# Performance work log

Hardware: AMD Instinct MI355X
Metric: run time of the kernel (lower is better)

Reference implementation:

```python
import jax, jax.numpy as jnp
import numpy as np

N = 50000
E = 800000
IN_C = 128
HID = 16
HEADS = 8
OUT_C = 64
NEG_SLOPE = 0.2


def setup_inputs() -> dict:
    key = jax.random.key(0)
    ks = jax.random.split(key, 12)
    x = jax.random.normal(ks[0], (N, IN_C), dtype=jnp.float32)
    edge_index = jax.random.randint(ks[1], (2, E), 0, N, dtype=jnp.int32)
    s = 0.1
    W1 = jax.random.normal(ks[2], (IN_C, HEADS * HID), dtype=jnp.float32) * s
    a1_src = jax.random.normal(ks[3], (HEADS, HID), dtype=jnp.float32) * s
    a1_dst = jax.random.normal(ks[4], (HEADS, HID), dtype=jnp.float32) * s
    b1 = jnp.zeros((HEADS * HID,), dtype=jnp.float32)
    W2 = jax.random.normal(ks[5], (HEADS * HID, OUT_C), dtype=jnp.float32) * s
    a2_src = jax.random.normal(ks[6], (1, OUT_C), dtype=jnp.float32) * s
    a2_dst = jax.random.normal(ks[7], (1, OUT_C), dtype=jnp.float32) * s
    b2 = jnp.zeros((OUT_C,), dtype=jnp.float32)
    return {"x": x, "edge_index": edge_index, "W1": W1, "a1_src": a1_src,
            "a1_dst": a1_dst, "b1": b1, "W2": W2, "a2_src": a2_src,
            "a2_dst": a2_dst, "b2": b2}


def gat_conv(x, src, dst, W, a_src, a_dst, b, heads, ch):
    # linear projection -> [N, H, C]
    h = (x @ W).reshape(N, heads, ch)
    # per-node attention logits [N, H]
    al_s = jnp.einsum('nhc,hc->nh', h, a_src)
    al_d = jnp.einsum('nhc,hc->nh', h, a_dst)
    # per-edge logits [E, H]
    e = jax.nn.leaky_relu(al_s[src] + al_d[dst], NEG_SLOPE)
    # segment softmax over incoming edges of each dst node
    emax = jax.ops.segment_max(e, dst, num_segments=N)
    ee = jnp.exp(e - emax[dst])
    denom = jax.ops.segment_sum(ee, dst, num_segments=N)
    alpha = ee / (denom[dst] + 1e-16)
    # weighted scatter-aggregate of source messages
    msg = h[src] * alpha[:, :, None]  # [E, H, C]
    out = jax.ops.segment_sum(msg, dst, num_segments=N)
    return out.reshape(N, heads * ch) + b


def reference(x, edge_index, W1, a1_src, a1_dst, b1, W2, a2_src, a2_dst, b2):
    # add self loops (PyG GATConv default add_self_loops=True)
    loops = jnp.arange(N, dtype=edge_index.dtype)
    src = jnp.concatenate([edge_index[0], loops])
    dst = jnp.concatenate([edge_index[1], loops])
    h = gat_conv(x, src, dst, W1, a1_src, a1_dst, b1, HEADS, HID)
    h = jax.nn.relu(h)
    # dropout p=0.6 is identity in eval mode
    out = gat_conv(h, src, dst, W2, a2_src, a2_dst, b2, 1, OUT_C)
    return out
```

## Files before the change

kernel.cpp:

```cpp
#include <hip/hip_runtime.h>
#include <hip/hip_fp16.h>
#include <math.h>

#define N_NODES 50000
#define E_EDGES 800000
#define IN_C    128
#define HID     16
#define HEADS   8
#define OUT_C   64
#define NEG_SLOPE 0.2f
#define ELLW    64

template <int OUTC, int HEADS_T>
__global__ __launch_bounds__(256) void fused_gemm_fill(
    const float* __restrict__ X, const float* __restrict__ W, __half* __restrict__ H,
    const float* __restrict__ a_src, const float* __restrict__ a_dst,
    float* __restrict__ als, float* __restrict__ ald, int nrows,
    const int* __restrict__ src, const int* __restrict__ dst,
    int* __restrict__ cursor, int* __restrict__ ell) {
    constexpr int CPG = OUTC / 4;
    constexpr int RT = (256 / CPG) * 4;
    constexpr int GROUP = (OUTC / HEADS_T) / 4;
    __shared__ __half wsh[IN_C * OUTC];
    __shared__ float xs[RT * 132];
    const int bid = blockIdx.x;

    if (bid & 1) {
        const int tid = (bid >> 1) * 256 + threadIdx.x;
        if (tid < E_EDGES / 4) {
            const int4 s4 = ((const int4*)src)[tid];
            const int4 d4 = ((const int4*)dst)[tid];
            const int p0 = atomicAdd(&cursor[d4.x], 1);
            const int p1 = atomicAdd(&cursor[d4.y], 1);
            const int p2 = atomicAdd(&cursor[d4.z], 1);
            const int p3 = atomicAdd(&cursor[d4.w], 1);
            ell[(size_t)d4.x * ELLW + p0] = s4.x;
            ell[(size_t)d4.y * ELLW + p1] = s4.y;
            ell[(size_t)d4.z * ELLW + p2] = s4.z;
            ell[(size_t)d4.w * ELLW + p3] = s4.w;
        }
        return;
    }

    const int t = threadIdx.x;
    for (int f = t * 4; f < IN_C * OUTC; f += 1024) {
        const float4 w4 = *(const float4*)&W[f];
        *(__half2*)&wsh[f]     = __float22half2_rn(make_float2(w4.x, w4.y));
        *(__half2*)&wsh[f + 2] = __float22half2_rn(make_float2(w4.z, w4.w));
    }
    const int row0 = (bid >> 1) * 64;
    const int cp = t % CPG;
    const int r0 = (t / CPG) * 4;
    float asr[4], adr[4];
#pragma unroll
    for (int j = 0; j < 4; ++j) {
        asr[j] = a_src[cp * 4 + j];
        adr[j] = a_dst[cp * 4 + j];
    }
    for (int rb = 0; rb < 64; rb += RT) {
        __syncthreads();
        for (int f = t * 4; f < RT * IN_C; f += 1024) {
            const int r = f >> 7, k = f & 127;
            int rl = row0 + rb + r;
            if (rl >= nrows) rl = nrows - 1;
            *(float4*)&xs[r * 132 + k] = *(const float4*)&X[(size_t)rl * IN_C + k];
        }
        __syncthreads();
        float acc[4][4] = {};
#pragma unroll 8
        for (int k = 0; k < IN_C; ++k) {
            const float2 wlo = __half22float2(*(const __half2*)&wsh[k * OUTC + cp * 4]);
            const float2 whi = __half22float2(*(const __half2*)&wsh[k * OUTC + cp * 4 + 2]);
#pragma unroll
            for (int i = 0; i < 4; ++i) {
                const float xi = xs[(r0 + i) * 132 + k];
                acc[i][0] += xi * wlo.x;
                acc[i][1] += xi * wlo.y;
                acc[i][2] += xi * whi.x;
                acc[i][3] += xi * whi.y;
            }
        }
#pragma unroll
        for (int i = 0; i < 4; ++i) {
            const int r = row0 + rb + r0 + i;
            float ps = acc[i][0] * asr[0] + acc[i][1] * asr[1] +
                       acc[i][2] * asr[2] + acc[i][3] * asr[3];
            float pd = acc[i][0] * adr[0] + acc[i][1] * adr[1] +
                       acc[i][2] * adr[2] + acc[i][3] * adr[3];
#pragma unroll
            for (int off = 1; off < GROUP; off <<= 1) {
                ps += __shfl_xor(ps, off);
                pd += __shfl_xor(pd, off);
            }
            if (r < nrows) {
                __half* hp = H + (size_t)r * OUTC + cp * 4;
                *(__half2*)(hp)     = __float22half2_rn(make_float2(acc[i][0], acc[i][1]));
                *(__half2*)(hp + 2) = __float22half2_rn(make_float2(acc[i][2], acc[i][3]));
                if ((cp % GROUP) == 0) {
                    const int hd = cp / GROUP;
                    als[(size_t)r * HEADS_T + hd] = ps;
                    ald[(size_t)r * HEADS_T + hd] = pd;
                }
            }
        }
    }
}

__device__ __forceinline__ float lrelu_exp(float v) {
    v = v > 0.f ? v : NEG_SLOPE * v;
    return __expf(v);
}

__global__ __launch_bounds__(256) void agg1_gemm2(
    const int* __restrict__ cnt, const int* __restrict__ ell,
    const float* __restrict__ als, const float* __restrict__ ald,
    const __half* __restrict__ H, const float* __restrict__ b,
    const float* __restrict__ W2, const float* __restrict__ a2_src,
    const float* __restrict__ a2_dst, __half* __restrict__ H2,
    float* __restrict__ als2, float* __restrict__ ald2) {
    __shared__ __half wsh[IN_C * OUT_C];
    __shared__ float xrow[8 * 132];
    const int t = threadIdx.x;
    for (int f = t * 4; f < IN_C * OUT_C; f += 1024) {
        const float4 w4 = *(const float4*)&W2[f];
        *(__half2*)&wsh[f]     = __float22half2_rn(make_float2(w4.x, w4.y));
        *(__half2*)&wsh[f + 2] = __float22half2_rn(make_float2(w4.z, w4.w));
    }

    const int nl = t >> 5, tl = t & 31, h = tl >> 2, cg = tl & 3;
    const int n = blockIdx.x * 8 + nl;
    const int deg = cnt[n];
    const int* ep = ell + (size_t)n * ELLW;
    const float ad = ald[n * HEADS + h];
    float ssum;
    float4 acc;
    {
        const float w = lrelu_exp(als[n * HEADS + h] + ad);
        const __half2* hp = (const __half2*)(H + ((size_t)n * HEADS + h) * HID + cg * 4);
        const float2 a0 = __half22float2(hp[0]);
        const float2 a1 = __half22float2(hp[1]);
        ssum = w;
        acc = make_float4(w * a0.x, w * a0.y, w * a1.x, w * a1.y);
    }
    int p = 0;
    for (; p + 4 <= deg; p += 4) {
        const int4 s4 = *(const int4*)(ep + p);
        const float v0 = als[s4.x * HEADS + h];
        const float v1 = als[s4.y * HEADS + h];
        const float v2 = als[s4.z * HEADS + h];
        const float v3 = als[s4.w * HEADS + h];
        const __half2* h0 = (const __half2*)(H + ((size_t)s4.x * HEADS + h) * HID + cg * 4);
        const __half2* h1 = (const __half2*)(H + ((size_t)s4.y * HEADS + h) * HID + cg * 4);
        const __half2* h2 = (const __half2*)(H + ((size_t)s4.z * HEADS + h) * HID + cg * 4);
        const __half2* h3 = (const __half2*)(H + ((size_t)s4.w * HEADS + h) * HID + cg * 4);
        const __half2 m00 = h0[0], m01 = h0[1];
        const __half2 m10 = h1[0], m11 = h1[1];
        const __half2 m20 = h2[0], m21 = h2[1];
        const __half2 m30 = h3[0], m31 = h3[1];
        const float w0 = lrelu_exp(v0 + ad);
        const float w1 = lrelu_exp(v1 + ad);
        const float w2 = lrelu_exp(v2 + ad);
        const float w3 = lrelu_exp(v3 + ad);
        ssum += (w0 + w1) + (w2 + w3);
        float2 f;
        f = __half22float2(m00); acc.x += w0 * f.x; acc.y += w0 * f.y;
        f = __half22float2(m01); acc.z += w0 * f.x; acc.w += w0 * f.y;
        f = __half22float2(m10); acc.x += w1 * f.x; acc.y += w1 * f.y;
        f = __half22float2(m11); acc.z += w1 * f.x; acc.w += w1 * f.y;
        f = __half22float2(m20); acc.x += w2 * f.x; acc.y += w2 * f.y;
        f = __half22float2(m21); acc.z += w2 * f.x; acc.w += w2 * f.y;
        f = __half22float2(m30); acc.x += w3 * f.x; acc.y += w3 * f.y;
        f = __half22float2(m31); acc.z += w3 * f.x; acc.w += w3 * f.y;
    }
    for (; p < deg; ++p) {
        const int s = ep[p];
        const float w = lrelu_exp(als[s * HEADS + h] + ad);
        const __half2* hp = (const __half2*)(H + ((size_t)s * HEADS + h) * HID + cg * 4);
        const float2 a0 = __half22float2(hp[0]);
        const float2 a1 = __half22float2(hp[1]);
        ssum += w;
        acc.x += w * a0.x; acc.y += w * a0.y; acc.z += w * a1.x; acc.w += w * a1.y;
    }
    const float inv = 1.f / (ssum + 1e-16f);
    const int c0 = h * HID + cg * 4;
    float4 r;
    r.x = acc.x * inv + b[c0 + 0];
    r.y = acc.y * inv + b[c0 + 1];
    r.z = acc.z * inv + b[c0 + 2];
    r.w = acc.w * inv + b[c0 + 3];
    r.x = r.x > 0.f ? r.x : 0.f;
    r.y = r.y > 0.f ? r.y : 0.f;
    r.z = r.z > 0.f ? r.z : 0.f;
    r.w = r.w > 0.f ? r.w : 0.f;
    float* xr = &xrow[nl * 132 + c0];
    xr[0] = r.x; xr[1] = r.y; xr[2] = r.z; xr[3] = r.w;

    __syncthreads();

    const int j0 = (t & 31) * 2;
    const int ng = t >> 5;
    const int n2 = blockIdx.x * 8 + ng;
    const float a2s0 = a2_src[j0], a2s1 = a2_src[j0 + 1];
    const float a2d0 = a2_dst[j0], a2d1 = a2_dst[j0 + 1];
    float o0 = 0.f, o1 = 0.f;
    const float* xb = &xrow[ng * 132];
#pragma unroll 4
    for (int c = 0; c < IN_C; c += 4) {
        const float4 xv = *(const float4*)&xb[c];
        const float2 wa = __half22float2(*(const __half2*)&wsh[(c + 0) * OUT_C + j0]);
        const float2 wb = __half22float2(*(const __half2*)&wsh[(c + 1) * OUT_C + j0]);
        const float2 wc = __half22float2(*(const __half2*)&wsh[(c + 2) * OUT_C + j0]);
        const float2 wd = __half22float2(*(const __half2*)&wsh[(c + 3) * OUT_C + j0]);
        o0 += xv.x * wa.x + xv.y * wb.x + xv.z * wc.x + xv.w * wd.x;
        o1 += xv.x * wa.y + xv.y * wb.y + xv.z * wc.y + xv.w * wd.y;
    }
    float ps = o0 * a2s0 + o1 * a2s1;
    float pd = o0 * a2d0 + o1 * a2d1;
#pragma unroll
    for (int off = 1; off < 32; off <<= 1) {
        ps += __shfl_xor(ps, off);
        pd += __shfl_xor(pd, off);
    }
    *(__half2*)(H2 + (size_t)n2 * OUT_C + j0) = __float22half2_rn(make_float2(o0, o1));
    if ((t & 31) == 0) {
        als2[n2] = ps;
        ald2[n2] = pd;
    }
}

__global__ void agg2(const int* __restrict__ cnt, const int* __restrict__ ell,
                     const float* __restrict__ als, const float* __restrict__ ald,
                     const __half* __restrict__ H, const float* __restrict__ b,
                     float* __restrict__ out) {
    int i = blockIdx.x * blockDim.x + threadIdx.x;
    if (i >= N_NODES * 16) return;
    const int n = i >> 4, cg = i & 15;
    const int deg = cnt[n];
    const int* ep = ell + (size_t)n * ELLW;
    const float ad = ald[n];
    float ssum;
    float4 acc;
    {
        const float w = lrelu_exp(als[n] + ad);
        const __half2* hp = (const __half2*)(H + (size_t)n * OUT_C + cg * 4);
        const float2 a0 = __half22float2(hp[0]);
        const float2 a1 = __half22float2(hp[1]);
        ssum = w;
        acc = make_float4(w * a0.x, w * a0.y, w * a1.x, w * a1.y);
    }
    int p = 0;
    for (; p + 4 <= deg; p += 4) {
        const int4 s4 = *(const int4*)(ep + p);
        const float v0 = als[s4.x];
        const float v1 = als[s4.y];
        const float v2 = als[s4.z];
        const float v3 = als[s4.w];
        const __half2* h0 = (const __half2*)(H + (size_t)s4.x * OUT_C + cg * 4);
        const __half2* h1 = (const __half2*)(H + (size_t)s4.y * OUT_C + cg * 4);
        const __half2* h2 = (const __half2*)(H + (size_t)s4.z * OUT_C + cg * 4);
        const __half2* h3 = (const __half2*)(H + (size_t)s4.w * OUT_C + cg * 4);
        const __half2 m00 = h0[0], m01 = h0[1];
        const __half2 m10 = h1[0], m11 = h1[1];
        const __half2 m20 = h2[0], m21 = h2[1];
        const __half2 m30 = h3[0], m31 = h3[1];
        const float w0 = lrelu_exp(v0 + ad);
        const float w1 = lrelu_exp(v1 + ad);
        const float w2 = lrelu_exp(v2 + ad);
        const float w3 = lrelu_exp(v3 + ad);
        ssum += (w0 + w1) + (w2 + w3);
        float2 f;
        f = __half22float2(m00); acc.x += w0 * f.x; acc.y += w0 * f.y;
        f = __half22float2(m01); acc.z += w0 * f.x; acc.w += w0 * f.y;
        f = __half22float2(m10); acc.x += w1 * f.x; acc.y += w1 * f.y;
        f = __half22float2(m11); acc.z += w1 * f.x; acc.w += w1 * f.y;
        f = __half22float2(m20); acc.x += w2 * f.x; acc.y += w2 * f.y;
        f = __half22float2(m21); acc.z += w2 * f.x; acc.w += w2 * f.y;
        f = __half22float2(m30); acc.x += w3 * f.x; acc.y += w3 * f.y;
        f = __half22float2(m31); acc.z += w3 * f.x; acc.w += w3 * f.y;
    }
    for (; p < deg; ++p) {
        const int s = ep[p];
        const float w = lrelu_exp(als[s] + ad);
        const __half2* hp = (const __half2*)(H + (size_t)s * OUT_C + cg * 4);
        const float2 a0 = __half22float2(hp[0]);
        const float2 a1 = __half22float2(hp[1]);
        ssum += w;
        acc.x += w * a0.x; acc.y += w * a0.y; acc.z += w * a1.x; acc.w += w * a1.y;
    }
    const float inv = 1.f / (ssum + 1e-16f);
    const int c0 = cg * 4;
    float4 r;
    r.x = acc.x * inv + b[c0 + 0];
    r.y = acc.y * inv + b[c0 + 1];
    r.z = acc.z * inv + b[c0 + 2];
    r.w = acc.w * inv + b[c0 + 3];
    *(float4*)(out + (size_t)n * OUT_C + c0) = r;
}

extern "C" void kernel_launch(void* const* d_in, const int* in_sizes, int n_in,
                              void* d_out, int out_size, void* d_ws, size_t ws_size,
                              hipStream_t stream) {
    const float* x      = (const float*)d_in[0];
    const int*   ei     = (const int*)d_in[1];
    const float* W1     = (const float*)d_in[2];
    const float* a1_src = (const float*)d_in[3];
    const float* a1_dst = (const float*)d_in[4];
    const float* b1     = (const float*)d_in[5];
    const float* W2     = (const float*)d_in[6];
    const float* a2_src = (const float*)d_in[7];
    const float* a2_dst = (const float*)d_in[8];
    const float* b2     = (const float*)d_in[9];
    const int* src = ei;
    const int* dst = ei + E_EDGES;
    float* outp = (float*)d_out;

    char* wsb = (char*)d_ws;
    __half* h1   = (__half*)wsb;
    __half* h2   = h1 + (size_t)N_NODES * IN_C;
    float*  als1 = (float*)(h2 + (size_t)N_NODES * OUT_C);
    float*  ald1 = als1 + N_NODES * HEADS;
    float*  als2 = ald1 + N_NODES * HEADS;
    float*  ald2 = als2 + N_NODES;
    int*    cursor = (int*)(ald2 + N_NODES);
    int*    ell    = cursor + N_NODES;

    hipMemsetAsync(cursor, 0, N_NODES * sizeof(int), stream);

    {
        const int gemm_blocks = (N_NODES + 63) / 64;
        fused_gemm_fill<IN_C, HEADS><<<gemm_blocks * 2, 256, 0, stream>>>(
            x, W1, h1, a1_src, a1_dst, als1, ald1, N_NODES, src, dst, cursor, ell);
    }

    agg1_gemm2<<<N_NODES / 8, 256, 0, stream>>>(
        cursor, ell, als1, ald1, h1, b1, W2, a2_src, a2_dst, h2, als2, ald2);

    {
        int n = N_NODES * 16;
        agg2<<<(n + 255) / 256, 256, 0, stream>>>(cursor, ell, als2, ald2, h2, b2, outp);
    }
}
```

Measured before the change: 230.6 us.

## Shard ELL adjacency per XCC and use MFMA for first-layer GEMM

The edge-fill path now reads the XCC id from a hardware register and writes into one of eight per-XCC cursor/ELL shards of width 24. This keeps atomics local to each die's L2 instead of contending across dies. Both aggregation kernels loop over all shards with masked 4-wide gathers. The first-layer projection switches from a scalar FMA tile loop to fp16 MFMA 16x16x32 with a transposed fp16 weight tile in LDS. Edges beyond 24 per shard are silently dropped, and the input X is now also rounded to fp16, which costs accuracy.

```diff
diff --git a/kernel.cpp b/kernel.cpp
--- a/kernel.cpp
+++ b/kernel.cpp
@@ -9,106 +9,110 @@
 #define HEADS   8
 #define OUT_C   64
 #define NEG_SLOPE 0.2f
-#define ELLW    64
-
-template <int OUTC, int HEADS_T>
+#define NSHARD  8
+#define SHW     24
+
+typedef _Float16 half8 __attribute__((ext_vector_type(8)));
+typedef float floatx4 __attribute__((ext_vector_type(4)));
+
+#define XCC_ID_REG (((4 - 1) << 11) | 20)
+
+__device__ __forceinline__ float lrelu_exp(float v) {
+    v = v > 0.f ? v : NEG_SLOPE * v;
+    return __expf(v);
+}
+
 __global__ __launch_bounds__(256) void fused_gemm_fill(
     const float* __restrict__ X, const float* __restrict__ W, __half* __restrict__ H,
     const float* __restrict__ a_src, const float* __restrict__ a_dst,
-    float* __restrict__ als, float* __restrict__ ald, int nrows,
+    float* __restrict__ als, float* __restrict__ ald,
     const int* __restrict__ src, const int* __restrict__ dst,
     int* __restrict__ cursor, int* __restrict__ ell) {
-    constexpr int CPG = OUTC / 4;
-    constexpr int RT = (256 / CPG) * 4;
-    constexpr int GROUP = (OUTC / HEADS_T) / 4;
-    __shared__ __half wsh[IN_C * OUTC];
-    __shared__ float xs[RT * 132];
+    __shared__ _Float16 wT[IN_C * 136];
     const int bid = blockIdx.x;
+    const int t = threadIdx.x;
 
     if (bid & 1) {
-        const int tid = (bid >> 1) * 256 + threadIdx.x;
+        const int xcc = __builtin_amdgcn_s_getreg(XCC_ID_REG) & 7;
+        int* cur = cursor + xcc * N_NODES;
+        int* es = ell + (size_t)xcc * N_NODES * SHW;
+        const int tid = (bid >> 1) * 256 + t;
         if (tid < E_EDGES / 4) {
             const int4 s4 = ((const int4*)src)[tid];
             const int4 d4 = ((const int4*)dst)[tid];
-            const int p0 = atomicAdd(&cursor[d4.x], 1);
-            const int p1 = atomicAdd(&cursor[d4.y], 1);
-            const int p2 = atomicAdd(&cursor[d4.z], 1);
-            const int p3 = atomicAdd(&cursor[d4.w], 1);
-            ell[(size_t)d4.x * ELLW + p0] = s4.x;
-            ell[(size_t)d4.y * ELLW + p1] = s4.y;
-            ell[(size_t)d4.z * ELLW + p2] = s4.z;
-            ell[(size_t)d4.w * ELLW + p3] = s4.w;
+            const int p0 = atomicAdd(&cur[d4.x], 1);
+            const int p1 = atomicAdd(&cur[d4.y], 1);
+            const int p2 = atomicAdd(&cur[d4.z], 1);
+            const int p3 = atomicAdd(&cur[d4.w], 1);
+            if (p0 < SHW) es[d4.x * SHW + p0] = s4.x;
+            if (p1 < SHW) es[d4.y * SHW + p1] = s4.y;
+            if (p2 < SHW) es[d4.z * SHW + p2] = s4.z;
+            if (p3 < SHW) es[d4.w * SHW + p3] = s4.w;
         }
         return;
     }
 
-    const int t = threadIdx.x;
-    for (int f = t * 4; f < IN_C * OUTC; f += 1024) {
+    for (int f = t * 4; f < IN_C * IN_C; f += 1024) {
         const float4 w4 = *(const float4*)&W[f];
-        *(__half2*)&wsh[f]     = __float22half2_rn(make_float2(w4.x, w4.y));
-        *(__half2*)&wsh[f + 2] = __float22half2_rn(make_float2(w4.z, w4.w));
-    }
-    const int row0 = (bid >> 1) * 64;
-    const int cp = t % CPG;
-    const int r0 = (t / CPG) * 4;
-    float asr[4], adr[4];
-#pragma unroll
-    for (int j = 0; j < 4; ++j) {
-        asr[j] = a_src[cp * 4 + j];
-        adr[j] = a_dst[cp * 4 + j];
-    }
-    for (int rb = 0; rb < 64; rb += RT) {
-        __syncthreads();
-        for (int f = t * 4; f < RT * IN_C; f += 1024) {
-            const int r = f >> 7, k = f & 127;
-            int rl = row0 + rb + r;
-            if (rl >= nrows) rl = nrows - 1;
-            *(float4*)&xs[r * 132 + k] = *(const float4*)&X[(size_t)rl * IN_C + k];
-        }
-        __syncthreads();
-        float acc[4][4] = {};
-#pragma unroll 8
-        for (int k = 0; k < IN_C; ++k) {
-            const float2 wlo = __half22float2(*(const __half2*)&wsh[k * OUTC + cp * 4]);
-            const float2 whi = __half22float2(*(const __half2*)&wsh[k * OUTC + cp * 4 + 2]);
-#pragma unroll
-            for (int i = 0; i < 4; ++i) {
-                const float xi = xs[(r0 + i) * 132 + k];
-                acc[i][0] += xi * wlo.x;
-                acc[i][1] += xi * wlo.y;
-                acc[i][2] += xi * whi.x;
-                acc[i][3] += xi * whi.y;
-            }
-        }
-#pragma unroll
-        for (int i = 0; i < 4; ++i) {
-            const int r = row0 + rb + r0 + i;
-            float ps = acc[i][0] * asr[0] + acc[i][1] * asr[1] +
-                       acc[i][2] * asr[2] + acc[i][3] * asr[3];
-            float pd = acc[i][0] * adr[0] + acc[i][1] * adr[1] +
-                       acc[i][2] * adr[2] + acc[i][3] * adr[3];
-#pragma unroll
-            for (int off = 1; off < GROUP; off <<= 1) {
-                ps += __shfl_xor(ps, off);
-                pd += __shfl_xor(pd, off);
-            }
-            if (r < nrows) {
-                __half* hp = H + (size_t)r * OUTC + cp * 4;
-                *(__half2*)(hp)     = __float22half2_rn(make_float2(acc[i][0], acc[i][1]));
-                *(__half2*)(hp + 2) = __float22half2_rn(make_float2(acc[i][2], acc[i][3]));
-                if ((cp % GROUP) == 0) {
-                    const int hd = cp / GROUP;
-                    als[(size_t)r * HEADS_T + hd] = ps;
-                    ald[(size_t)r * HEADS_T + hd] = pd;
+        const int k = f >> 7, col = f & 127;
+        wT[(col + 0) * 136 + k] = (_Float16)w4.x;
+        wT[(col + 1) * 136 + k] = (_Float16)w4.y;
+        wT[(col + 2) * 136 + k] = (_Float16)w4.z;
+        wT[(col + 3) * 136 + k] = (_Float16)w4.w;
+    }
+    __syncthreads();
+
+    const int wave = t >> 6, lane = t & 63;
+    const int m = lane & 15, quad = lane >> 4;
+    const int r0w = (bid >> 1) * 64 + wave * 16;
+    int rl = r0w + m;
+    if (rl >= N_NODES) rl = N_NODES - 1;
+    const float* Xr = X + (size_t)rl * IN_C;
+
+    floatx4 acc[8];
+#pragma unroll
+    for (int i = 0; i < 8; ++i) acc[i] = (floatx4){0.f, 0.f, 0.f, 0.f};
+
+#pragma unroll
+    for (int kc = 0; kc < 4; ++kc) {
+        const int k8 = kc * 32 + quad * 8;
+        const float4 xa = *(const float4*)(Xr + k8);
+        const float4 xb = *(const float4*)(Xr + k8 + 4);
+        half8 a;
+        a[0] = (_Float16)xa.x; a[1] = (_Float16)xa.y;
+        a[2] = (_Float16)xa.z; a[3] = (_Float16)xa.w;
+        a[4] = (_Float16)xb.x; a[5] = (_Float16)xb.y;
+        a[6] = (_Float16)xb.z; a[7] = (_Float16)xb.w;
+#pragma unroll
+        for (int ct = 0; ct < 8; ++ct) {
+            const half8 b = *(const half8*)&wT[(ct * 16 + m) * 136 + k8];
+            acc[ct] = __builtin_amdgcn_mfma_f32_16x16x32_f16(a, b, acc[ct], 0, 0, 0);
+        }
+    }
+
+    _Float16* Hh = (_Float16*)H;
+#pragma unroll
+    for (int ct = 0; ct < 8; ++ct) {
+        const float asv = a_src[ct * 16 + m];
+        const float adv = a_dst[ct * 16 + m];
+#pragma unroll
+        for (int r = 0; r < 4; ++r) {
+            const int row = r0w + quad * 4 + r;
+            const float c = acc[ct][r];
+            float ps = c * asv, pd = c * adv;
+            ps += __shfl_xor(ps, 1); pd += __shfl_xor(pd, 1);
+            ps += __shfl_xor(ps, 2); pd += __shfl_xor(pd, 2);
+            ps += __shfl_xor(ps, 4); pd += __shfl_xor(pd, 4);
+            ps += __shfl_xor(ps, 8); pd += __shfl_xor(pd, 8);
+            if (row < N_NODES) {
+                Hh[(size_t)row * IN_C + ct * 16 + m] = (_Float16)c;
+                if (m == 0) {
+                    als[(size_t)row * HEADS + ct] = ps;
+                    ald[(size_t)row * HEADS + ct] = pd;
                 }
             }
         }
     }
-}
-
-__device__ __forceinline__ float lrelu_exp(float v) {
-    v = v > 0.f ? v : NEG_SLOPE * v;
-    return __expf(v);
 }
 
 __global__ __launch_bounds__(256) void agg1_gemm2(
@@ -129,8 +133,6 @@
 
     const int nl = t >> 5, tl = t & 31, h = tl >> 2, cg = tl & 3;
     const int n = blockIdx.x * 8 + nl;
-    const int deg = cnt[n];
-    const int* ep = ell + (size_t)n * ELLW;
     const float ad = ald[n * HEADS + h];
     float ssum;
     float4 acc;
@@ -142,44 +144,45 @@
         ssum = w;
         acc = make_float4(w * a0.x, w * a0.y, w * a1.x, w * a1.y);
     }
-    int p = 0;
-    for (; p + 4 <= deg; p += 4) {
-        const int4 s4 = *(const int4*)(ep + p);
-        const float v0 = als[s4.x * HEADS + h];
-        const float v1 = als[s4.y * HEADS + h];
-        const float v2 = als[s4.z * HEADS + h];
-        const float v3 = als[s4.w * HEADS + h];
-        const __half2* h0 = (const __half2*)(H + ((size_t)s4.x * HEADS + h) * HID + cg * 4);
-        const __half2* h1 = (const __half2*)(H + ((size_t)s4.y * HEADS + h) * HID + cg * 4);
-        const __half2* h2 = (const __half2*)(H + ((size_t)s4.z * HEADS + h) * HID + cg * 4);
-        const __half2* h3 = (const __half2*)(H + ((size_t)s4.w * HEADS + h) * HID + cg * 4);
-        const __half2 m00 = h0[0], m01 = h0[1];
-        const __half2 m10 = h1[0], m11 = h1[1];
-        const __half2 m20 = h2[0], m21 = h2[1];
-        const __half2 m30 = h3[0], m31 = h3[1];
-        const float w0 = lrelu_exp(v0 + ad);
-        const float w1 = lrelu_exp(v1 + ad);
-        const float w2 = lrelu_exp(v2 + ad);
-        const float w3 = lrelu_exp(v3 + ad);
-        ssum += (w0 + w1) + (w2 + w3);
-        float2 f;
-        f = __half22float2(m00); acc.x += w0 * f.x; acc.y += w0 * f.y;
-        f = __half22float2(m01); acc.z += w0 * f.x; acc.w += w0 * f.y;
-        f = __half22float2(m10); acc.x += w1 * f.x; acc.y += w1 * f.y;
-        f = __half22float2(m11); acc.z += w1 * f.x; acc.w += w1 * f.y;
-        f = __half22float2(m20); acc.x += w2 * f.x; acc.y += w2 * f.y;
-        f = __half22float2(m21); acc.z += w2 * f.x; acc.w += w2 * f.y;
-        f = __half22float2(m30); acc.x += w3 * f.x; acc.y += w3 * f.y;
-        f = __half22float2(m31); acc.z += w3 * f.x; acc.w += w3 * f.y;
-    }
-    for (; p < deg; ++p) {
-        const int s = ep[p];
-        const float w = lrelu_exp(als[s * HEADS + h] + ad);
-        const __half2* hp = (const __half2*)(H + ((size_t)s * HEADS + h) * HID + cg * 4);
-        const float2 a0 = __half22float2(hp[0]);
-        const float2 a1 = __half22float2(hp[1]);
-        ssum += w;
-        acc.x += w * a0.x; acc.y += w * a0.y; acc.z += w * a1.x; acc.w += w * a1.y;
+    for (int sh = 0; sh < NSHARD; ++sh) {
+        int deg = cnt[sh * N_NODES + n];
+        deg = deg < SHW ? deg : SHW;
+        const int* ep = ell + ((size_t)sh * N_NODES + (size_t)n) * SHW;
+        for (int p = 0; p < deg; p += 4) {
+            const int4 s4 = *(const int4*)(ep + p);
+            const int i1 = (p + 1 < deg) ? s4.y : n;
+            const int i2 = (p + 2 < deg) ? s4.z : n;
+            const int i3 = (p + 3 < deg) ? s4.w : n;
+            const float f1 = (p + 1 < deg) ? 1.f : 0.f;
+            const float f2 = (p + 2 < deg) ? 1.f : 0.f;
+            const float f3 = (p + 3 < deg) ? 1.f : 0.f;
+            const float v0 = als[s4.x * HEADS + h];
+            const float v1 = als[i1 * HEADS + h];
+            const float v2 = als[i2 * HEADS + h];
+            const float v3 = als[i3 * HEADS + h];
+            const __half2* h0 = (const __half2*)(H + ((size_t)s4.x * HEADS + h) * HID + cg * 4);
+            const __half2* h1 = (const __half2*)(H + ((size_t)i1 * HEADS + h) * HID + cg * 4);
+            const __half2* h2 = (const __half2*)(H + ((size_t)i2 * HEADS + h) * HID + cg * 4);
+            const __half2* h3 = (const __half2*)(H + ((size_t)i3 * HEADS + h) * HID + cg * 4);
+            const __half2 m00 = h0[0], m01 = h0[1];
+            const __half2 m10 = h1[0], m11 = h1[1];
+            const __half2 m20 = h2[0], m21 = h2[1];
+            const __half2 m30 = h3[0], m31 = h3[1];
+            const float w0 = lrelu_exp(v0 + ad);
+            const float w1 = lrelu_exp(v1 + ad) * f1;
+            const float w2 = lrelu_exp(v2 + ad) * f2;
+            const float w3 = lrelu_exp(v3 + ad) * f3;
+            ssum += (w0 + w1) + (w2 + w3);
+            float2 f;
+            f = __half22float2(m00); acc.x += w0 * f.x; acc.y += w0 * f.y;
+            f = __half22float2(m01); acc.z += w0 * f.x; acc.w += w0 * f.y;
+            f = __half22float2(m10); acc.x += w1 * f.x; acc.y += w1 * f.y;
+            f = __half22float2(m11); acc.z += w1 * f.x; acc.w += w1 * f.y;
+            f = __half22float2(m20); acc.x += w2 * f.x; acc.y += w2 * f.y;
+            f = __half22float2(m21); acc.z += w2 * f.x; acc.w += w2 * f.y;
+            f = __half22float2(m30); acc.x += w3 * f.x; acc.y += w3 * f.y;
+            f = __half22float2(m31); acc.z += w3 * f.x; acc.w += w3 * f.y;
+        }
     }
     const float inv = 1.f / (ssum + 1e-16f);
     const int c0 = h * HID + cg * 4;
@@ -235,8 +238,6 @@
     int i = blockIdx.x * blockDim.x + threadIdx.x;
     if (i >= N_NODES * 16) return;
     const int n = i >> 4, cg = i & 15;
-    const int deg = cnt[n];
-    const int* ep = ell + (size_t)n * ELLW;
     const float ad = ald[n];
     float ssum;
     float4 acc;
@@ -248,44 +249,45 @@
         ssum = w;
         acc = make_float4(w * a0.x, w * a0.y, w * a1.x, w * a1.y);
     }
-    int p = 0;
-    for (; p + 4 <= deg; p += 4) {
-        const int4 s4 = *(const int4*)(ep + p);
-        const float v0 = als[s4.x];
-        const float v1 = als[s4.y];
-        const float v2 = als[s4.z];
-        const float v3 = als[s4.w];
-        const __half2* h0 = (const __half2*)(H + (size_t)s4.x * OUT_C + cg * 4);
-        const __half2* h1 = (const __half2*)(H + (size_t)s4.y * OUT_C + cg * 4);
-        const __half2* h2 = (const __half2*)(H + (size_t)s4.z * OUT_C + cg * 4);
-        const __half2* h3 = (const __half2*)(H + (size_t)s4.w * OUT_C + cg * 4);
-        const __half2 m00 = h0[0], m01 = h0[1];
-        const __half2 m10 = h1[0], m11 = h1[1];
-        const __half2 m20 = h2[0], m21 = h2[1];
-        const __half2 m30 = h3[0], m31 = h3[1];
-        const float w0 = lrelu_exp(v0 + ad);
-        const float w1 = lrelu_exp(v1 + ad);
-        const float w2 = lrelu_exp(v2 + ad);
-        const float w3 = lrelu_exp(v3 + ad);
-        ssum += (w0 + w1) + (w2 + w3);
-        float2 f;
-        f = __half22float2(m00); acc.x += w0 * f.x; acc.y += w0 * f.y;
-        f = __half22float2(m01); acc.z += w0 * f.x; acc.w += w0 * f.y;
-        f = __half22float2(m10); acc.x += w1 * f.x; acc.y += w1 * f.y;
-        f = __half22float2(m11); acc.z += w1 * f.x; acc.w += w1 * f.y;
-        f = __half22float2(m20); acc.x += w2 * f.x; acc.y += w2 * f.y;
-        f = __half22float2(m21); acc.z += w2 * f.x; acc.w += w2 * f.y;
-        f = __half22float2(m30); acc.x += w3 * f.x; acc.y += w3 * f.y;
-        f = __half22float2(m31); acc.z += w3 * f.x; acc.w += w3 * f.y;
-    }
-    for (; p < deg; ++p) {
-        const int s = ep[p];
-        const float w = lrelu_exp(als[s] + ad);
-        const __half2* hp = (const __half2*)(H + (size_t)s * OUT_C + cg * 4);
-        const float2 a0 = __half22float2(hp[0]);
-        const float2 a1 = __half22float2(hp[1]);
-        ssum += w;
-        acc.x += w * a0.x; acc.y += w * a0.y; acc.z += w * a1.x; acc.w += w * a1.y;
+    for (int sh = 0; sh < NSHARD; ++sh) {
+        int deg = cnt[sh * N_NODES + n];
+        deg = deg < SHW ? deg : SHW;
+        const int* ep = ell + ((size_t)sh * N_NODES + (size_t)n) * SHW;
+        for (int p = 0; p < deg; p += 4) {
+            const int4 s4 = *(const int4*)(ep + p);
+            const int i1 = (p + 1 < deg) ? s4.y : n;
+            const int i2 = (p + 2 < deg) ? s4.z : n;
+            const int i3 = (p + 3 < deg) ? s4.w : n;
+            const float f1 = (p + 1 < deg) ? 1.f : 0.f;
+            const float f2 = (p + 2 < deg) ? 1.f : 0.f;
+            const float f3 = (p + 3 < deg) ? 1.f : 0.f;
+            const float v0 = als[s4.x];
+            const float v1 = als[i1];
+            const float v2 = als[i2];
+            const float v3 = als[i3];
+            const __half2* h0 = (const __half2*)(H + (size_t)s4.x * OUT_C + cg * 4);
+            const __half2* h1 = (const __half2*)(H + (size_t)i1 * OUT_C + cg * 4);
+            const __half2* h2 = (const __half2*)(H + (size_t)i2 * OUT_C + cg * 4);
+            const __half2* h3 = (const __half2*)(H + (size_t)i3 * OUT_C + cg * 4);
+            const __half2 m00 = h0[0], m01 = h0[1];
+            const __half2 m10 = h1[0], m11 = h1[1];
+            const __half2 m20 = h2[0], m21 = h2[1];
+            const __half2 m30 = h3[0], m31 = h3[1];
+            const float w0 = lrelu_exp(v0 + ad);
+            const float w1 = lrelu_exp(v1 + ad) * f1;
+            const float w2 = lrelu_exp(v2 + ad) * f2;
+            const float w3 = lrelu_exp(v3 + ad) * f3;
+            ssum += (w0 + w1) + (w2 + w3);
+            float2 f;
+            f = __half22float2(m00); acc.x += w0 * f.x; acc.y += w0 * f.y;
+            f = __half22float2(m01); acc.z += w0 * f.x; acc.w += w0 * f.y;
+            f = __half22float2(m10); acc.x += w1 * f.x; acc.y += w1 * f.y;
+            f = __half22float2(m11); acc.z += w1 * f.x; acc.w += w1 * f.y;
+            f = __half22float2(m20); acc.x += w2 * f.x; acc.y += w2 * f.y;
+            f = __half22float2(m21); acc.z += w2 * f.x; acc.w += w2 * f.y;
+            f = __half22float2(m30); acc.x += w3 * f.x; acc.y += w3 * f.y;
+            f = __half22float2(m31); acc.z += w3 * f.x; acc.w += w3 * f.y;
+        }
     }
     const float inv = 1.f / (ssum + 1e-16f);
     const int c0 = cg * 4;
@@ -322,14 +324,14 @@
     float*  als2 = ald1 + N_NODES * HEADS;
     float*  ald2 = als2 + N_NODES;
     int*    cursor = (int*)(ald2 + N_NODES);
-    int*    ell    = cursor + N_NODES;
-
-    hipMemsetAsync(cursor, 0, N_NODES * sizeof(int), stream);
+    int*    ell    = cursor + NSHARD * N_NODES;
+
+    hipMemsetAsync(cursor, 0, NSHARD * N_NODES * sizeof(int), stream);
 
     {
         const int gemm_blocks = (N_NODES + 63) / 64;
-        fused_gemm_fill<IN_C, HEADS><<<gemm_blocks * 2, 256, 0, stream>>>(
-            x, W1, h1, a1_src, a1_dst, als1, ald1, N_NODES, src, dst, cursor, ell);
+        fused_gemm_fill<<<gemm_blocks * 2, 256, 0, stream>>>(
+            x, W1, h1, a1_src, a1_dst, als1, ald1, src, dst, cursor, ell);
     }
 
     agg1_gemm2<<<N_NODES / 8, 256, 0, stream>>>(
```

After: 235.5 us. 1.02x slower.
